# Optimization experiments

Hardware: AMD Instinct MI355X
Metric: run time of the kernel (lower is better)

The kernel has to match this reference:

```python
import jax, jax.numpy as jnp
import numpy as np

D_MODEL = 1024
N_HEADS = 16
HEAD_DIM = D_MODEL // N_HEADS


def setup_inputs() -> dict:
    key = jax.random.key(0)
    k1, k2, k3 = jax.random.split(key, 3)
    B, T = 4, 2048
    x = jax.random.normal(k1, (B, T, D_MODEL), dtype=jnp.float32)
    # match nn.Linear default init scale roughly (small weights for stability)
    w_qkv = jax.random.normal(k2, (D_MODEL, 3 * D_MODEL), dtype=jnp.float32) / np.sqrt(D_MODEL)
    w_proj = jax.random.normal(k3, (D_MODEL, D_MODEL), dtype=jnp.float32) / np.sqrt(D_MODEL)
    b_proj = jnp.zeros((D_MODEL,), dtype=jnp.float32)
    return {"x": x, "w_qkv": w_qkv, "w_proj": w_proj, "b_proj": b_proj}


def reference(x, w_qkv, w_proj, b_proj):
    B, T, C = x.shape
    qkv = x @ w_qkv  # [B,T,3C]
    q, k, v = jnp.split(qkv, 3, axis=-1)
    # [B, H, T, hd]
    q = q.reshape(B, T, N_HEADS, HEAD_DIM).transpose(0, 2, 1, 3)
    k = k.reshape(B, T, N_HEADS, HEAD_DIM).transpose(0, 2, 1, 3)
    v = v.reshape(B, T, N_HEADS, HEAD_DIM).transpose(0, 2, 1, 3)
    scale = 1.0 / np.sqrt(HEAD_DIM).astype(np.float32)
    att = jnp.einsum("bhqd,bhkd->bhqk", q, k) * scale
    causal = jnp.tril(jnp.ones((T, T), dtype=bool))
    att = jnp.where(causal[None, None], att, jnp.float32(-jnp.inf))
    att = jax.nn.softmax(att, axis=-1)
    # dropout p=0.0 (eval) -> identity
    out = jnp.einsum("bhqk,bhkd->bhqd", att, v)
    out = out.transpose(0, 2, 1, 3).reshape(B, T, C)
    return out @ w_proj + b_proj
```

## Files before the change

### kernel.cpp

```cpp
#include <hip/hip_runtime.h>
#include <stdint.h>

#define D_MODEL 1024
#define N_HEADS 16
#define HEAD_DIM 64
#define BATCH 4
#define SEQ 2048
#define ROWS (BATCH * SEQ)
#define K3 (3 * D_MODEL)
#define NQT (SEQ / 64)
#define SCALE_Q 0.1803368867f

typedef unsigned short u16;
typedef unsigned int u32;
typedef __attribute__((ext_vector_type(8))) short short8;
typedef __attribute__((ext_vector_type(4))) float floatx4;

typedef const __attribute__((address_space(1))) u32* gptr_t;
typedef __attribute__((address_space(3))) u32* lptr_t;

__device__ __forceinline__ float bf2f(u16 u) {
    return __uint_as_float(((unsigned)u) << 16);
}
__device__ __forceinline__ u16 f2b(float f) {
    unsigned u = __float_as_uint(f);
    u = u + 0x7fffu + ((u >> 16) & 1u);
    return (u16)(u >> 16);
}
__device__ __forceinline__ unsigned pk2(float a, float b) {
    return (unsigned)f2b(a) | ((unsigned)f2b(b) << 16);
}

__global__ __launch_bounds__(256) void conv_f2b4(const float* __restrict__ x,
                                                 u16* __restrict__ xb, int n4) {
    int i = blockIdx.x * 256 + threadIdx.x;
    if (i < n4) {
        float4 v = ((const float4*)x)[i];
        uint2 p;
        p.x = pk2(v.x, v.y);
        p.y = pk2(v.z, v.w);
        ((uint2*)xb)[i] = p;
    }
}

__global__ __launch_bounds__(256) void transpose_f2b(const float* __restrict__ w,
                                                     u16* __restrict__ wt,
                                                     int R, int C) {
    int idx = blockIdx.x * 256 + threadIdx.x;
    if (idx >= R * C) return;
    int r = idx / C, c = idx - r * C;
    wt[(size_t)c * R + r] = f2b(w[idx]);
}

__global__ __launch_bounds__(256) void transpose_v(const u16* __restrict__ v,
                                                   u16* __restrict__ vt) {
    const int bh = blockIdx.y;
    const int t = blockIdx.x * 256 + threadIdx.x;
    const u16* src = v + ((size_t)bh * SEQ + t) * HEAD_DIM;
    u16* dst = vt + (size_t)bh * HEAD_DIM * SEQ + t;
    #pragma unroll
    for (int d = 0; d < HEAD_DIM; ++d)
        dst[(size_t)d * SEQ] = src[d];
}

#define GEMM_CORE_GLD(KDIM)                                                    \
    __shared__ u16 As[128][64];                                                \
    __shared__ u16 Bs[128][64];                                                \
    const int tid  = threadIdx.x;                                              \
    const int wave = tid >> 6, lane = tid & 63;                                \
    const int quad = lane >> 4, l15 = lane & 15;                               \
    const int wr = wave >> 1, wc = wave & 1;                                   \
    const int m0 = blockIdx.y * 128, n0 = blockIdx.x * 128;                    \
    const int lrow8 = lane >> 3;                                               \
    const int csw = 8 * ((lane & 7) ^ lrow8);           \
    const int swA = (l15 & 7) * 8;                      \
    floatx4 acc[4][4] = {};                                                    \
    for (int k0 = 0; k0 < (KDIM); k0 += 64) {                                  \
        _Pragma("unroll")                                                      \
        for (int i = 0; i < 4; ++i) {                                          \
            const int rb = i * 32 + wave * 8;                                  \
            const int r  = rb + lrow8;                                         \
            __builtin_amdgcn_global_load_lds(                                  \
                (gptr_t)(A + (size_t)(m0 + r) * (KDIM) + k0 + csw),            \
                (lptr_t)(&As[rb][0]), 16, 0, 0);                               \
            __builtin_amdgcn_global_load_lds(                                  \
                (gptr_t)(Bt + (size_t)(n0 + r) * (KDIM) + k0 + csw),           \
                (lptr_t)(&Bs[rb][0]), 16, 0, 0);                               \
        }                                                                      \
        __syncthreads();                                                       \
        _Pragma("unroll")                                                      \
        for (int ks = 0; ks < 2; ++ks) {                                       \
            const int kk = ks * 32 + quad * 8;                                 \
            short8 af[4], bf[4];                                               \
            _Pragma("unroll")                                                  \
            for (int t = 0; t < 4; ++t) {                                      \
                af[t] = *(const short8*)&As[wr * 64 + t * 16 + l15][kk ^ swA]; \
                bf[t] = *(const short8*)&Bs[wc * 64 + t * 16 + l15][kk ^ swA]; \
            }                                                                  \
            _Pragma("unroll")                                                  \
            for (int i = 0; i < 4; ++i)                                        \
                _Pragma("unroll")                                              \
                for (int j = 0; j < 4; ++j)                                    \
                    acc[i][j] = __builtin_amdgcn_mfma_f32_16x16x32_bf16(       \
                        af[i], bf[j], acc[i][j], 0, 0, 0);                     \
        }                                                                      \
        __syncthreads();                                                       \
    }

__global__ __launch_bounds__(256) void gemm_qkv(const u16* __restrict__ A,
                                                const u16* __restrict__ Bt,
                                                u16* __restrict__ qo,
                                                u16* __restrict__ ko,
                                                u16* __restrict__ vo) {
    GEMM_CORE_GLD(D_MODEL)
    const int which = n0 >> 10;
    u16* dst = which == 0 ? qo : (which == 1 ? ko : vo);
    const float scl = which == 0 ? SCALE_Q : 1.f;
    #pragma unroll
    for (int i = 0; i < 4; ++i)
        #pragma unroll
        for (int j = 0; j < 4; ++j) {
            const int col = n0 + wc * 64 + j * 16 + l15;
            const int rb  = m0 + wr * 64 + i * 16 + quad * 4;
            const int cc  = col & 1023;
            const int h = cc >> 6, d = cc & 63;
            #pragma unroll
            for (int rr = 0; rr < 4; ++rr) {
                const int row = rb + rr;
                const int b = row >> 11, t = row & 2047;
                dst[(((size_t)(b * N_HEADS + h)) * SEQ + t) * HEAD_DIM + d] =
                    f2b(acc[i][j][rr] * scl);
            }
        }
}

__global__ __launch_bounds__(256) void gemm_proj(const u16* __restrict__ A,
                                                 const u16* __restrict__ Bt,
                                                 const float* __restrict__ bias,
                                                 float* __restrict__ out) {
    GEMM_CORE_GLD(D_MODEL)
    #pragma unroll
    for (int i = 0; i < 4; ++i)
        #pragma unroll
        for (int j = 0; j < 4; ++j) {
            const int col = n0 + wc * 64 + j * 16 + l15;
            const int rb  = m0 + wr * 64 + i * 16 + quad * 4;
            const float bv = bias[col];
            #pragma unroll
            for (int rr = 0; rr < 4; ++rr) {
                const int row = rb + rr;
                out[(size_t)row * D_MODEL + col] = acc[i][j][rr] + bv;
            }
        }
}

__global__ __launch_bounds__(256, 4) void attn_mfma(const u16* __restrict__ q,
                                                    const u16* __restrict__ k,
                                                    const u16* __restrict__ vt,
                                                    u16* __restrict__ o) {
    __shared__ u16 Ks[64][64];
    __shared__ u16 Vs[64][64];
    __shared__ u16 Plds[4][16][72];
    const int tid = threadIdx.x;
    const int w = tid >> 6, lane = tid & 63;
    const int quad = lane >> 4, l15 = lane & 15;
    const int bh = blockIdx.y;
    const int b = bh >> 4, h = bh & 15;
    const u16* kb  = k  + (size_t)bh * SEQ * HEAD_DIM;
    const u16* vtb = vt + (size_t)bh * HEAD_DIM * SEQ;
    const int lrow8 = lane >> 3;
    const int csw = 8 * ((lane & 7) ^ lrow8);
    const int swA = (l15 & 7) * 8;

    #pragma unroll 1
    for (int seg = 0; seg < 2; ++seg) {
        const int qt = seg ? (int)blockIdx.x : (NQT - 1 - (int)blockIdx.x);
        const int qrow = qt * 64 + w * 16 + l15;
        const u16* qp = q + ((size_t)bh * SEQ + qrow) * HEAD_DIM + quad * 8;
        const short8 bq0 = *(const short8*)(qp);
        const short8 bq1 = *(const short8*)(qp + 32);

        floatx4 O[4] = {};
        float l = 0.f;

        for (int c = 0; c <= qt; ++c) {
            __syncthreads();
            {
                const int r0 = w * 16 + lrow8;
                __builtin_amdgcn_global_load_lds(
                    (gptr_t)(kb + (size_t)(c * 64 + r0) * HEAD_DIM + csw),
                    (lptr_t)(&Ks[w * 16][0]), 16, 0, 0);
                __builtin_amdgcn_global_load_lds(
                    (gptr_t)(kb + (size_t)(c * 64 + r0 + 8) * HEAD_DIM + csw),
                    (lptr_t)(&Ks[w * 16 + 8][0]), 16, 0, 0);
                __builtin_amdgcn_global_load_lds(
                    (gptr_t)(vtb + (size_t)(r0) * SEQ + c * 64 + csw),
                    (lptr_t)(&Vs[w * 16][0]), 16, 0, 0);
                __builtin_amdgcn_global_load_lds(
                    (gptr_t)(vtb + (size_t)(r0 + 8) * SEQ + c * 64 + csw),
                    (lptr_t)(&Vs[w * 16 + 8][0]), 16, 0, 0);
            }
            __syncthreads();
            floatx4 s[4];
            #pragma unroll
            for (int kt = 0; kt < 4; ++kt) {
                short8 ak0 = *(const short8*)&Ks[kt * 16 + l15][(quad * 8) ^ swA];
                short8 ak1 = *(const short8*)&Ks[kt * 16 + l15][(32 + quad * 8) ^ swA];
                floatx4 z = {};
                z = __builtin_amdgcn_mfma_f32_16x16x32_bf16(ak0, bq0, z, 0, 0, 0);
                z = __builtin_amdgcn_mfma_f32_16x16x32_bf16(ak1, bq1, z, 0, 0, 0);
                s[kt] = z;
            }
            float e[4][4];
            #pragma unroll
            for (int kt = 0; kt < 4; ++kt)
                #pragma unroll
                for (int r = 0; r < 4; ++r)
                    e[kt][r] = exp2f(s[kt][r]);
            if (c == qt) {
                #pragma unroll
                for (int kt = 0; kt < 4; ++kt)
                    #pragma unroll
                    for (int r = 0; r < 4; ++r)
                        if (kt * 16 + quad * 4 + r > w * 16 + l15) e[kt][r] = 0.f;
            }
            float ls = 0.f;
            #pragma unroll
            for (int kt = 0; kt < 4; ++kt) {
                ls += (e[kt][0] + e[kt][1]) + (e[kt][2] + e[kt][3]);
                uint2 pkv;
                pkv.x = pk2(e[kt][0], e[kt][1]);
                pkv.y = pk2(e[kt][2], e[kt][3]);
                *(uint2*)&Plds[w][l15][kt * 16 + quad * 4] = pkv;
            }
            l += ls;
            short8 pb0 = *(const short8*)&Plds[w][l15][quad * 8];
            short8 pb1 = *(const short8*)&Plds[w][l15][32 + quad * 8];
            #pragma unroll
            for (int dt = 0; dt < 4; ++dt) {
                short8 av0 = *(const short8*)&Vs[dt * 16 + l15][(quad * 8) ^ swA];
                short8 av1 = *(const short8*)&Vs[dt * 16 + l15][(32 + quad * 8) ^ swA];
                O[dt] = __builtin_amdgcn_mfma_f32_16x16x32_bf16(av0, pb0, O[dt], 0, 0, 0);
                O[dt] = __builtin_amdgcn_mfma_f32_16x16x32_bf16(av1, pb1, O[dt], 0, 0, 0);
            }
        }
        l += __shfl_xor(l, 16);
        l += __shfl_xor(l, 32);
        const float inv = 1.f / l;
        u16* op = o + ((size_t)(b * SEQ + qrow)) * D_MODEL + h * 64 + quad * 4;
        #pragma unroll
        for (int dt = 0; dt < 4; ++dt) {
            uint2 pkv;
            pkv.x = pk2(O[dt][0] * inv, O[dt][1] * inv);
            pkv.y = pk2(O[dt][2] * inv, O[dt][3] * inv);
            *(uint2*)(op + dt * 16) = pkv;
        }
    }
}

extern "C" void kernel_launch(void* const* d_in, const int* in_sizes, int n_in,
                              void* d_out, int out_size, void* d_ws, size_t ws_size,
                              hipStream_t stream) {
    const float* x      = (const float*)d_in[0];
    const float* w_qkv  = (const float*)d_in[1];
    const float* w_proj = (const float*)d_in[2];
    const float* b_proj = (const float*)d_in[3];
    float* out = (float*)d_out;

    u16* xb      = (u16*)d_ws;
    u16* wt_qkv  = xb + (size_t)ROWS * D_MODEL;
    u16* wt_proj = wt_qkv + (size_t)D_MODEL * K3;
    u16* qws     = wt_proj + (size_t)D_MODEL * D_MODEL;
    u16* kws     = qws + (size_t)ROWS * D_MODEL;
    u16* vtws    = kws + (size_t)ROWS * D_MODEL;
    u16* aout    = vtws + (size_t)ROWS * D_MODEL;
    u16* vnat    = aout;

    conv_f2b4<<<(ROWS * D_MODEL / 4 + 255) / 256, 256, 0, stream>>>(x, xb, ROWS * D_MODEL / 4);
    transpose_f2b<<<(D_MODEL * K3 + 255) / 256, 256, 0, stream>>>(w_qkv, wt_qkv, D_MODEL, K3);
    transpose_f2b<<<(D_MODEL * D_MODEL + 255) / 256, 256, 0, stream>>>(w_proj, wt_proj, D_MODEL, D_MODEL);

    gemm_qkv<<<dim3(K3 / 128, ROWS / 128), 256, 0, stream>>>(xb, wt_qkv, qws, kws, vnat);

    transpose_v<<<dim3(SEQ / 256, BATCH * N_HEADS), 256, 0, stream>>>(vnat, vtws);

    attn_mfma<<<dim3(NQT / 2, BATCH * N_HEADS), 256, 0, stream>>>(qws, kws, vtws, aout);

    gemm_proj<<<dim3(D_MODEL / 128, ROWS / 128), 256, 0, stream>>>(aout, wt_proj, b_proj, out);
}
```

Measured before the change: 290.9 us.

## Tile transposes via LDS and double-buffer K/V tiles in attention

The weight and V transposes now stage 64x64 tiles in padded shared memory, so both global reads and writes are coalesced instead of writing with large strides. The attention kernel double-buffers its K and V shared tiles and prefetches the next chunk while computing the current one, cutting one barrier per iteration. It also replaces the padding on the P staging buffer with an XOR swizzle to avoid bank conflicts. The cost is doubled LDS use in attention, which may lower occupancy, and reliance on the barrier to wait for the async LDS loads to finish.

```diff
diff --git a/kernel.cpp b/kernel.cpp
--- a/kernel.cpp
+++ b/kernel.cpp
@@ -43,24 +43,45 @@
     }
 }
 
-__global__ __launch_bounds__(256) void transpose_f2b(const float* __restrict__ w,
-                                                     u16* __restrict__ wt,
-                                                     int R, int C) {
-    int idx = blockIdx.x * 256 + threadIdx.x;
-    if (idx >= R * C) return;
-    int r = idx / C, c = idx - r * C;
-    wt[(size_t)c * R + r] = f2b(w[idx]);
-}
-
-__global__ __launch_bounds__(256) void transpose_v(const u16* __restrict__ v,
-                                                   u16* __restrict__ vt) {
+__global__ __launch_bounds__(256) void transpose_f2b_t(const float* __restrict__ w,
+                                                       u16* __restrict__ wt,
+                                                       int R, int C) {
+    __shared__ u16 tile[64][65];
+    const int tx = threadIdx.x & 63;
+    const int ty = threadIdx.x >> 6;
+    const int r0 = blockIdx.y * 64, c0 = blockIdx.x * 64;
+    #pragma unroll
+    for (int i = 0; i < 16; ++i) {
+        const int r = i * 4 + ty;
+        tile[r][tx] = f2b(w[(size_t)(r0 + r) * C + c0 + tx]);
+    }
+    __syncthreads();
+    #pragma unroll
+    for (int i = 0; i < 16; ++i) {
+        const int c = i * 4 + ty;
+        wt[(size_t)(c0 + c) * R + r0 + tx] = tile[tx][c];
+    }
+}
+
+__global__ __launch_bounds__(256) void transpose_v2(const u16* __restrict__ v,
+                                                    u16* __restrict__ vt) {
+    __shared__ u16 tile[64][65];
     const int bh = blockIdx.y;
-    const int t = blockIdx.x * 256 + threadIdx.x;
-    const u16* src = v + ((size_t)bh * SEQ + t) * HEAD_DIM;
-    u16* dst = vt + (size_t)bh * HEAD_DIM * SEQ + t;
-    #pragma unroll
-    for (int d = 0; d < HEAD_DIM; ++d)
-        dst[(size_t)d * SEQ] = src[d];
+    const int t0 = blockIdx.x * 64;
+    const int tx = threadIdx.x & 63, ty = threadIdx.x >> 6;
+    const u16* src = v + ((size_t)bh * SEQ + t0) * HEAD_DIM;
+    #pragma unroll
+    for (int i = 0; i < 16; ++i) {
+        const int r = i * 4 + ty;
+        tile[r][tx] = src[r * HEAD_DIM + tx];
+    }
+    __syncthreads();
+    u16* dst = vt + (size_t)bh * HEAD_DIM * SEQ + t0;
+    #pragma unroll
+    for (int i = 0; i < 16; ++i) {
+        const int d = i * 4 + ty;
+        dst[(size_t)d * SEQ + tx] = tile[tx][d];
+    }
 }
 
 #define GEMM_CORE_GLD(KDIM)                                                    \
@@ -158,9 +179,9 @@
                                                     const u16* __restrict__ k,
                                                     const u16* __restrict__ vt,
                                                     u16* __restrict__ o) {
-    __shared__ u16 Ks[64][64];
-    __shared__ u16 Vs[64][64];
-    __shared__ u16 Plds[4][16][72];
+    __shared__ u16 Ks[2][64][64];
+    __shared__ u16 Vs[2][64][64];
+    __shared__ u16 Plds[4][16][64];
     const int tid = threadIdx.x;
     const int w = tid >> 6, lane = tid & 63;
     const int quad = lane >> 4, l15 = lane & 15;
@@ -171,6 +192,7 @@
     const int lrow8 = lane >> 3;
     const int csw = 8 * ((lane & 7) ^ lrow8);
     const int swA = (l15 & 7) * 8;
+    const int r0 = w * 16 + lrow8;
 
     #pragma unroll 1
     for (int seg = 0; seg < 2; ++seg) {
@@ -183,29 +205,43 @@
         floatx4 O[4] = {};
         float l = 0.f;
 
+        __syncthreads();
+        __builtin_amdgcn_global_load_lds(
+            (gptr_t)(kb + (size_t)(r0) * HEAD_DIM + csw),
+            (lptr_t)(&Ks[0][w * 16][0]), 16, 0, 0);
+        __builtin_amdgcn_global_load_lds(
+            (gptr_t)(kb + (size_t)(r0 + 8) * HEAD_DIM + csw),
+            (lptr_t)(&Ks[0][w * 16 + 8][0]), 16, 0, 0);
+        __builtin_amdgcn_global_load_lds(
+            (gptr_t)(vtb + (size_t)(r0) * SEQ + csw),
+            (lptr_t)(&Vs[0][w * 16][0]), 16, 0, 0);
+        __builtin_amdgcn_global_load_lds(
+            (gptr_t)(vtb + (size_t)(r0 + 8) * SEQ + csw),
+            (lptr_t)(&Vs[0][w * 16 + 8][0]), 16, 0, 0);
+
         for (int c = 0; c <= qt; ++c) {
+            const int cb = c & 1;
             __syncthreads();
-            {
-                const int r0 = w * 16 + lrow8;
+            if (c < qt) {
+                const int nb = cb ^ 1;
                 __builtin_amdgcn_global_load_lds(
-                    (gptr_t)(kb + (size_t)(c * 64 + r0) * HEAD_DIM + csw),
-                    (lptr_t)(&Ks[w * 16][0]), 16, 0, 0);
+                    (gptr_t)(kb + (size_t)((c + 1) * 64 + r0) * HEAD_DIM + csw),
+                    (lptr_t)(&Ks[nb][w * 16][0]), 16, 0, 0);
                 __builtin_amdgcn_global_load_lds(
-                    (gptr_t)(kb + (size_t)(c * 64 + r0 + 8) * HEAD_DIM + csw),
-                    (lptr_t)(&Ks[w * 16 + 8][0]), 16, 0, 0);
+                    (gptr_t)(kb + (size_t)((c + 1) * 64 + r0 + 8) * HEAD_DIM + csw),
+                    (lptr_t)(&Ks[nb][w * 16 + 8][0]), 16, 0, 0);
                 __builtin_amdgcn_global_load_lds(
-                    (gptr_t)(vtb + (size_t)(r0) * SEQ + c * 64 + csw),
-                    (lptr_t)(&Vs[w * 16][0]), 16, 0, 0);
+                    (gptr_t)(vtb + (size_t)(r0) * SEQ + (c + 1) * 64 + csw),
+                    (lptr_t)(&Vs[nb][w * 16][0]), 16, 0, 0);
                 __builtin_amdgcn_global_load_lds(
-                    (gptr_t)(vtb + (size_t)(r0 + 8) * SEQ + c * 64 + csw),
-                    (lptr_t)(&Vs[w * 16 + 8][0]), 16, 0, 0);
-            }
-            __syncthreads();
+                    (gptr_t)(vtb + (size_t)(r0 + 8) * SEQ + (c + 1) * 64 + csw),
+                    (lptr_t)(&Vs[nb][w * 16 + 8][0]), 16, 0, 0);
+            }
             floatx4 s[4];
             #pragma unroll
             for (int kt = 0; kt < 4; ++kt) {
-                short8 ak0 = *(const short8*)&Ks[kt * 16 + l15][(quad * 8) ^ swA];
-                short8 ak1 = *(const short8*)&Ks[kt * 16 + l15][(32 + quad * 8) ^ swA];
+                short8 ak0 = *(const short8*)&Ks[cb][kt * 16 + l15][(quad * 8) ^ swA];
+                short8 ak1 = *(const short8*)&Ks[cb][kt * 16 + l15][(32 + quad * 8) ^ swA];
                 floatx4 z = {};
                 z = __builtin_amdgcn_mfma_f32_16x16x32_bf16(ak0, bq0, z, 0, 0, 0);
                 z = __builtin_amdgcn_mfma_f32_16x16x32_bf16(ak1, bq1, z, 0, 0, 0);
@@ -231,15 +267,15 @@
                 uint2 pkv;
                 pkv.x = pk2(e[kt][0], e[kt][1]);
                 pkv.y = pk2(e[kt][2], e[kt][3]);
-                *(uint2*)&Plds[w][l15][kt * 16 + quad * 4] = pkv;
+                *(uint2*)&Plds[w][l15][(kt * 16 + quad * 4) ^ swA] = pkv;
             }
             l += ls;
-            short8 pb0 = *(const short8*)&Plds[w][l15][quad * 8];
-            short8 pb1 = *(const short8*)&Plds[w][l15][32 + quad * 8];
+            short8 pb0 = *(const short8*)&Plds[w][l15][(quad * 8) ^ swA];
+            short8 pb1 = *(const short8*)&Plds[w][l15][(32 + quad * 8) ^ swA];
             #pragma unroll
             for (int dt = 0; dt < 4; ++dt) {
-                short8 av0 = *(const short8*)&Vs[dt * 16 + l15][(quad * 8) ^ swA];
-                short8 av1 = *(const short8*)&Vs[dt * 16 + l15][(32 + quad * 8) ^ swA];
+                short8 av0 = *(const short8*)&Vs[cb][dt * 16 + l15][(quad * 8) ^ swA];
+                short8 av1 = *(const short8*)&Vs[cb][dt * 16 + l15][(32 + quad * 8) ^ swA];
                 O[dt] = __builtin_amdgcn_mfma_f32_16x16x32_bf16(av0, pb0, O[dt], 0, 0, 0);
                 O[dt] = __builtin_amdgcn_mfma_f32_16x16x32_bf16(av1, pb1, O[dt], 0, 0, 0);
             }
@@ -277,12 +313,12 @@
     u16* vnat    = aout;
 
     conv_f2b4<<<(ROWS * D_MODEL / 4 + 255) / 256, 256, 0, stream>>>(x, xb, ROWS * D_MODEL / 4);
-    transpose_f2b<<<(D_MODEL * K3 + 255) / 256, 256, 0, stream>>>(w_qkv, wt_qkv, D_MODEL, K3);
-    transpose_f2b<<<(D_MODEL * D_MODEL + 255) / 256, 256, 0, stream>>>(w_proj, wt_proj, D_MODEL, D_MODEL);
+    transpose_f2b_t<<<dim3(K3 / 64, D_MODEL / 64), 256, 0, stream>>>(w_qkv, wt_qkv, D_MODEL, K3);
+    transpose_f2b_t<<<dim3(D_MODEL / 64, D_MODEL / 64), 256, 0, stream>>>(w_proj, wt_proj, D_MODEL, D_MODEL);
 
     gemm_qkv<<<dim3(K3 / 128, ROWS / 128), 256, 0, stream>>>(xb, wt_qkv, qws, kws, vnat);
 
-    transpose_v<<<dim3(SEQ / 256, BATCH * N_HEADS), 256, 0, stream>>>(vnat, vtws);
+    transpose_v2<<<dim3(SEQ / 64, BATCH * N_HEADS), 256, 0, stream>>>(vnat, vtws);
 
     attn_mfma<<<dim3(NQT / 2, BATCH * N_HEADS), 256, 0, stream>>>(qws, kws, vtws, aout);
 
```

After: 272.3 us. -6.4%, faster.
